# Optimization experiments

Measured on AMD Instinct MI355X. Metric: run time of the kernel, lower is better.

The kernel has to match this reference:

```python
import jax, jax.numpy as jnp
import numpy as np

N, X_DIM, Z_DIM, H = 4096, 256, 128, 512
NUM_ACTIONS = 4
TEMPERATURE = 0.1


def _init_linear(key, fan_in, fan_out):
    kw, kb = jax.random.split(key)
    bound = 1.0 / np.sqrt(fan_in)
    W = jax.random.uniform(kw, (fan_in, fan_out), minval=-bound, maxval=bound, dtype=jnp.float32)
    b = jax.random.uniform(kb, (fan_out,), minval=-bound, maxval=bound, dtype=jnp.float32)
    return W, b


def setup_inputs() -> dict:
    key = jax.random.key(0)
    ks = jax.random.split(key, 9)
    s = jax.random.normal(ks[0], (N, X_DIM), dtype=jnp.float32)
    sp = jax.random.normal(ks[1], (N, X_DIM), dtype=jnp.float32)
    a = jax.random.randint(ks[2], (N,), 0, NUM_ACTIONS)
    a1h = jax.nn.one_hot(a, NUM_ACTIONS, dtype=jnp.float32)
    # phi: x_dim -> 512 -> 512 -> z_dim
    pW0, pb0 = _init_linear(ks[3], X_DIM, H)
    pW1, pb1 = _init_linear(ks[4], H, H)
    pW2, pb2 = _init_linear(ks[5], H, Z_DIM)
    # g: x_dim + 4 -> 512 -> 512 -> z_dim
    gW0, gb0 = _init_linear(ks[6], X_DIM + NUM_ACTIONS, H)
    gW1, gb1 = _init_linear(ks[7], H, H)
    gW2, gb2 = _init_linear(ks[8], H, Z_DIM)
    return {"s": s, "sp": sp, "a1h": a1h,
            "pW0": pW0, "pb0": pb0, "pW1": pW1, "pb1": pb1, "pW2": pW2, "pb2": pb2,
            "gW0": gW0, "gb0": gb0, "gW1": gW1, "gb1": gb1, "gW2": gW2, "gb2": gb2}


def _mlp(x, W0, b0, W1, b1, W2, b2):
    h = jax.nn.relu(x @ W0 + b0)
    h = jax.nn.relu(h @ W1 + b1)
    return h @ W2 + b2


def reference(s, sp, a1h, pW0, pb0, pW1, pb1, pW2, pb2, gW0, gb0, gW1, gb1, gW2, gb2):
    z = _mlp(s, pW0, pb0, pW1, pb1, pW2, pb2)                      # [N, D]
    zpos = _mlp(jnp.concatenate([sp, a1h], axis=-1), gW0, gb0, gW1, gb1, gW2, gb2)  # [N, D]
    # -||z_i - zpos_j||^2 / T via the GEMM trick (avoids the [N,N,D] diff tensor)
    sq_z = jnp.sum(z * z, axis=-1, keepdims=True)                  # [N, 1]
    sq_p = jnp.sum(zpos * zpos, axis=-1)                            # [N]
    logits = -(sq_z + sq_p[None, :] - 2.0 * z @ zpos.T) / TEMPERATURE  # [N, N]
    # cross-entropy with targets = arange(N): diagonal is the positive
    log_probs = jax.nn.log_softmax(logits, axis=-1)
    loss = -jnp.mean(jnp.diagonal(log_probs))
    return loss
```

## Files before the change

### kernel.cpp

```cpp
#include <hip/hip_runtime.h>
#include <math.h>

#define NR 4096
#define ZD 128
#define HD 512
#define NJR 32
#define INV_T 10.0f

typedef __attribute__((ext_vector_type(8))) short bf16x8;
typedef __attribute__((ext_vector_type(4))) short short4v;
typedef __attribute__((ext_vector_type(4))) float f32x4;

typedef const unsigned int __attribute__((address_space(1)))* gas_t;
typedef unsigned int __attribute__((address_space(3)))* las_t;

__device__ __forceinline__ unsigned short f2bf(float f) {
  union { float f; unsigned u; } v; v.f = f;
  unsigned r = v.u + 0x7fff + ((v.u >> 16) & 1);
  return (unsigned short)(r >> 16);
}
__device__ __forceinline__ float bf2f(unsigned short b) {
  union { unsigned u; float f; } v; v.u = ((unsigned)b) << 16;
  return v.f;
}


__global__ __launch_bounds__(256) void prep(
    const float* __restrict__ s, const float* __restrict__ sp,
    const float* __restrict__ a1h,
    unsigned short* __restrict__ Sb, unsigned short* __restrict__ SPb,
    int* __restrict__ aidx,
    const float* __restrict__ pW0, unsigned short* __restrict__ pW0t,
    const float* __restrict__ pW1, unsigned short* __restrict__ pW1t,
    const float* __restrict__ pW2, unsigned short* __restrict__ pW2t,
    const float* __restrict__ gW0, unsigned short* __restrict__ gW0t,
    const float* __restrict__ gW1, unsigned short* __restrict__ gW1t,
    const float* __restrict__ gW2, unsigned short* __restrict__ gW2t,
    float* __restrict__ out) {
  int b = blockIdx.x, tid = threadIdx.x;
  if (b < 16) {
    int r = b * 256 + tid;
    int a = 0;
#pragma unroll
    for (int j = 0; j < 4; ++j) if (a1h[(size_t)r * 4 + j] > 0.5f) a = j;
    aidx[r] = a;
    if (b == 0 && tid == 0) out[0] = 0.f;
    return;
  }
  const int idx8 = tid & 127;
  const int h = idx8 & 1, p = idx8 >> 1, hi = p >> 4, l15 = p & 15;
  if (b < 2064) {
    const float* src = (b < 1040) ? s : sp;
    unsigned short* dst = (b < 1040) ? Sb : SPb;
    int lb = (b < 1040) ? b - 16 : b - 1040;
    int s0 = lb * 2 + (tid >> 7);
    int rf = s0 >> 3, ks = s0 & 7;
    int row = rf * 16 + l15, c0 = ks * 32 + hi * 4 + h * 16;
    float4 v = *(const float4*)&src[(size_t)row * 256 + c0];
    short4v o = { (short)f2bf(v.x), (short)f2bf(v.y), (short)f2bf(v.z), (short)f2bf(v.w) };
    *(short4v*)((char*)dst + (size_t)s0 * 1024 + idx8 * 8) = o;
    return;
  }
  int local = b - 2064;
  const float* W; unsigned short* Wt; int N, ksh;
  if (local < 128)      { W = pW0; Wt = pW0t; N = 512; ksh = 3; }
  else if (local < 384) { W = pW1; Wt = pW1t; N = 512; ksh = 4; local -= 128; }
  else if (local < 448) { W = pW2; Wt = pW2t; N = 128; ksh = 4; local -= 384; }
  else if (local < 576) { W = gW0; Wt = gW0t; N = 512; ksh = 3; local -= 448; }
  else if (local < 832) { W = gW1; Wt = gW1t; N = 512; ksh = 4; local -= 576; }
  else                  { W = gW2; Wt = gW2t; N = 128; ksh = 4; local -= 832; }
  int s0 = local * 2 + (tid >> 7);
  int rf = s0 >> ksh, ks = s0 & ((1 << ksh) - 1);
  int n = rf * 16 + l15, k0 = ks * 32 + hi * 4 + h * 16;
  short4v o = { (short)f2bf(W[(size_t)(k0 + 0) * N + n]),
                (short)f2bf(W[(size_t)(k0 + 1) * N + n]),
                (short)f2bf(W[(size_t)(k0 + 2) * N + n]),
                (short)f2bf(W[(size_t)(k0 + 3) * N + n]) };
  *(short4v*)((char*)Wt + (size_t)s0 * 1024 + idx8 * 8) = o;
}

template <int BM, int K, bool RELU, bool GB, bool SQ>
__global__ __launch_bounds__(256) void gemm_p3(
    const unsigned short* __restrict__ A0, const unsigned short* __restrict__ A1,
    const unsigned short* __restrict__ W0, const unsigned short* __restrict__ W1,
    const float* __restrict__ b0, const float* __restrict__ b1,
    unsigned short* __restrict__ C0, unsigned short* __restrict__ C1,
    float* __restrict__ sqp2, int N,
    const int* __restrict__ aidx, const float* __restrict__ gW0f) {
  constexpr int KS = K >> 5;
  constexpr int NSTEP = K >> 6;
  constexpr int ABYTES = BM * 128;
  constexpr int BBYTES = 8192;
  constexpr int NA = BM >> 5;
  constexpr int WM_FR = BM >> 5;
  constexpr int V = NA + 2;
  __shared__ char lds[3 * (ABYTES + BBYTES)];
  char* AsB = lds;
  char* BsB = lds + 3 * ABYTES;

  const int tid = threadIdx.x, lane = tid & 63, w = tid >> 6;
  const int wm = w >> 1, wn = w & 1;
  const int z = blockIdx.z;
  const char* Ab = (const char*)(z ? A1 : A0);
  const char* Wb = (const char*)(z ? W1 : W0);
  const float* bias = z ? b1 : b0;
  char* Cb = (char*)(z ? C1 : C0);
  const int bm = blockIdx.x * BM, bn = blockIdx.y * 64;
  const int lane16 = lane * 16;

  auto stage = [&](int buf, int st) {
#pragma unroll
    for (int u = 0; u < NA; ++u) {
      const int sl = w * NA + u;
      const char* src = Ab + ((size_t)((bm >> 4) + (sl >> 1)) * KS + st * 2 + (sl & 1)) * 1024 + lane16;
      __builtin_amdgcn_global_load_lds((gas_t)src, (las_t)(AsB + buf * ABYTES + sl * 1024), 16, 0, 0);
    }
#pragma unroll
    for (int u = 0; u < 2; ++u) {
      const int sl = w * 2 + u;
      const char* src = Wb + ((size_t)((bn >> 4) + (sl >> 1)) * KS + st * 2 + (sl & 1)) * 1024 + lane16;
      __builtin_amdgcn_global_load_lds((gas_t)src, (las_t)(BsB + buf * BBYTES + sl * 1024), 16, 0, 0);
    }
  };

  f32x4 acc[WM_FR][2] = {};
  stage(0, 0);
  stage(1, 1);
#pragma unroll
  for (int st = 0; st < NSTEP; ++st) {
    const int buf = st % 3;
    if (st + 2 < NSTEP) {
      stage((st + 2) % 3, st + 2);
      if constexpr (V == 6) asm volatile("s_waitcnt vmcnt(12)" ::: "memory");
      else                  asm volatile("s_waitcnt vmcnt(8)" ::: "memory");
    } else if (st + 1 < NSTEP) {
      if constexpr (V == 6) asm volatile("s_waitcnt vmcnt(6)" ::: "memory");
      else                  asm volatile("s_waitcnt vmcnt(4)" ::: "memory");
    } else {
      asm volatile("s_waitcnt vmcnt(0)" ::: "memory");
    }
    __builtin_amdgcn_s_barrier();
#pragma unroll
    for (int kss = 0; kss < 2; ++kss) {
      bf16x8 af[WM_FR], bfv[2];
#pragma unroll
      for (int i = 0; i < WM_FR; ++i)
        af[i] = *(const bf16x8*)(AsB + buf * ABYTES + ((wm * WM_FR + i) * 2 + kss) * 1024 + lane16);
#pragma unroll
      for (int j = 0; j < 2; ++j)
        bfv[j] = *(const bf16x8*)(BsB + buf * BBYTES + ((wn * 2 + j) * 2 + kss) * 1024 + lane16);
#pragma unroll
      for (int i = 0; i < WM_FR; ++i)
#pragma unroll
        for (int j = 0; j < 2; ++j)
          acc[i][j] = __builtin_amdgcn_mfma_f32_16x16x32_bf16(bfv[j], af[i], acc[i][j], 0, 0, 0);
    }
    __builtin_amdgcn_s_barrier();
  }

  const int l15 = lane & 15, hi = lane >> 4;
  const int NS = N >> 5;
  const int row0 = bm + wm * (BM / 2);
  const int col0 = bn + wn * 32;
  float sq[WM_FR];
  int ar[WM_FR];
#pragma unroll
  for (int i = 0; i < WM_FR; ++i) { sq[i] = 0.f; ar[i] = 0; }
  if (GB && z == 1) {
#pragma unroll
    for (int i = 0; i < WM_FR; ++i) ar[i] = aidx[row0 + i * 16 + l15];
  }
  float4 bi0 = *(const float4*)&bias[col0 + hi * 4];
  float4 bi1 = *(const float4*)&bias[col0 + 16 + hi * 4];
#pragma unroll
  for (int i = 0; i < WM_FR; ++i) {
    const int rfC = (row0 >> 4) + i;
    float v[8] = { acc[i][0][0] + bi0.x, acc[i][0][1] + bi0.y,
                   acc[i][0][2] + bi0.z, acc[i][0][3] + bi0.w,
                   acc[i][1][0] + bi1.x, acc[i][1][1] + bi1.y,
                   acc[i][1][2] + bi1.z, acc[i][1][3] + bi1.w };
    if (GB && z == 1) {
      float4 g0 = *(const float4*)&gW0f[(size_t)(256 + ar[i]) * N + col0 + hi * 4];
      float4 g1 = *(const float4*)&gW0f[(size_t)(256 + ar[i]) * N + col0 + 16 + hi * 4];
      v[0] += g0.x; v[1] += g0.y; v[2] += g0.z; v[3] += g0.w;
      v[4] += g1.x; v[5] += g1.y; v[6] += g1.z; v[7] += g1.w;
    }
    bf16x8 r;
#pragma unroll
    for (int t = 0; t < 8; ++t) {
      float vv = RELU ? fmaxf(v[t], 0.f) : v[t];
      unsigned short cv = f2bf(vv);
      r[t] = (short)cv;
      if (SQ) { float vb = bf2f(cv); sq[i] += vb * vb; }
    }
    *(bf16x8*)(Cb + (size_t)(rfC * NS + (col0 >> 5)) * 1024 + lane16) = r;
  }
  if (SQ && z == 1) {
#pragma unroll
    for (int i = 0; i < WM_FR; ++i) {
      float t = sq[i];
      t += __shfl_xor(t, 16, 64);
      t += __shfl_xor(t, 32, 64);
      if (lane < 16) sqp2[(size_t)(col0 >> 5) * NR + row0 + i * 16 + lane] = t;
    }
  }
}

__global__ __launch_bounds__(256) void logits_fm(
    const unsigned short* __restrict__ Zb, const unsigned short* __restrict__ Zpb,
    const float* __restrict__ sqp2, float* __restrict__ wm_,
    float* __restrict__ wsum, float* __restrict__ wdiag) {
  const int tid = threadIdx.x, lane = tid & 63, w = tid >> 6;
  const int l15 = lane & 15, hi = lane >> 4;
  const int i0 = blockIdx.x * 128, jr = blockIdx.y;
  const int row32 = i0 + w * 32;
  const int jbase = jr * 128;
  const int lane16 = lane * 16;
  const char* Zc = (const char*)Zb;
  const char* Pc = (const char*)Zpb;

  bf16x8 afr[2][4];
#pragma unroll
  for (int rf = 0; rf < 2; ++rf)
#pragma unroll
    for (int ks = 0; ks < 4; ++ks)
      afr[rf][ks] = *(const bf16x8*)(Zc + (size_t)(((row32 >> 4) + rf) * 4 + ks) * 1024 + lane16);

  f32x4 acc[2][8] = {};
#pragma unroll
  for (int jf = 0; jf < 8; ++jf) {
    const size_t js = (size_t)((jbase >> 4) + jf) * 4;
#pragma unroll
    for (int ks = 0; ks < 4; ++ks) {
      bf16x8 bfv = *(const bf16x8*)(Pc + (js + ks) * 1024 + lane16);
      acc[0][jf] = __builtin_amdgcn_mfma_f32_16x16x32_bf16(bfv, afr[0][ks], acc[0][jf], 0, 0, 0);
      acc[1][jf] = __builtin_amdgcn_mfma_f32_16x16x32_bf16(bfv, afr[1][ks], acc[1][jf], 0, 0, 0);
    }
  }

#pragma unroll
  for (int rf = 0; rf < 2; ++rf) {
    const int grow = row32 + rf * 16 + l15;
    float mx = -INFINITY, dd = 0.f;
    bool hasd = false;
#pragma unroll
    for (int jf = 0; jf < 8; ++jf) {
      const int cb = jbase + jf * 16 + hi * 4;
      float4 q0 = *(const float4*)&sqp2[cb];
      float4 q1 = *(const float4*)&sqp2[NR + cb];
      float4 q2 = *(const float4*)&sqp2[2 * NR + cb];
      float4 q3 = *(const float4*)&sqp2[3 * NR + cb];
      float sp[4] = { q0.x + q1.x + q2.x + q3.x, q0.y + q1.y + q2.y + q3.y,
                      q0.z + q1.z + q2.z + q3.z, q0.w + q1.w + q2.w + q3.w };
#pragma unroll
      for (int e = 0; e < 4; ++e) {
        float lv = (2.f * acc[rf][jf][e] - sp[e]) * INV_T;
        acc[rf][jf][e] = lv;
        mx = fmaxf(mx, lv);
        if (cb + e == grow) { dd = lv; hasd = true; }
      }
    }
    mx = fmaxf(mx, __shfl_xor(mx, 16, 64));
    mx = fmaxf(mx, __shfl_xor(mx, 32, 64));
    float sum = 0.f;
#pragma unroll
    for (int jf = 0; jf < 8; ++jf)
#pragma unroll
      for (int e = 0; e < 4; ++e) sum += __expf(acc[rf][jf][e] - mx);
    sum += __shfl_xor(sum, 16, 64);
    sum += __shfl_xor(sum, 32, 64);
    if (hi == 0) {
      wm_[(size_t)jr * NR + grow] = mx;
      wsum[(size_t)jr * NR + grow] = sum;
    }
    if (hasd) wdiag[grow] = dd;
  }
}

__global__ __launch_bounds__(256) void finalize(const float* __restrict__ wm,
    const float* __restrict__ wsum, const float* __restrict__ wdiag,
    float* __restrict__ out) {
  int r = blockIdx.x * 256 + threadIdx.x;
  float mm = wm[r];
  float ss = wsum[r];
#pragma unroll
  for (int p = 1; p < NJR; ++p) {
    float mo = wm[(size_t)p * NR + r];
    float so = wsum[(size_t)p * NR + r];
    float mn = fmaxf(mm, mo);
    ss = ss * __expf(mm - mn) + so * __expf(mo - mn);
    mm = mn;
  }
  float loss_r = mm + logf(ss) - wdiag[r];
  float v = loss_r;
#pragma unroll
  for (int off = 32; off; off >>= 1) v += __shfl_xor(v, off, 64);
  __shared__ float partial[4];
  if ((threadIdx.x & 63) == 0) partial[threadIdx.x >> 6] = v;
  __syncthreads();
  if (threadIdx.x == 0)
    atomicAdd(out, (partial[0] + partial[1] + partial[2] + partial[3]) * (1.0f / (float)NR));
}

extern "C" void kernel_launch(void* const* d_in, const int* in_sizes, int n_in,
                              void* d_out, int out_size, void* d_ws, size_t ws_size,
                              hipStream_t stream) {
  const float* s   = (const float*)d_in[0];
  const float* sp  = (const float*)d_in[1];
  const float* a1h = (const float*)d_in[2];
  const float* pW0 = (const float*)d_in[3];
  const float* pb0 = (const float*)d_in[4];
  const float* pW1 = (const float*)d_in[5];
  const float* pb1 = (const float*)d_in[6];
  const float* pW2 = (const float*)d_in[7];
  const float* pb2 = (const float*)d_in[8];
  const float* gW0 = (const float*)d_in[9];
  const float* gb0 = (const float*)d_in[10];
  const float* gW1 = (const float*)d_in[11];
  const float* gb1 = (const float*)d_in[12];
  const float* gW2 = (const float*)d_in[13];
  const float* gb2 = (const float*)d_in[14];

  char* p = (char*)d_ws;
  unsigned short* Sb   = (unsigned short*)p; p += (size_t)NR * 256 * 2;
  unsigned short* SPb  = (unsigned short*)p; p += (size_t)NR * 256 * 2;
  unsigned short* H1   = (unsigned short*)p; p += (size_t)2 * NR * HD * 2;
  unsigned short* H2   = (unsigned short*)p; p += (size_t)2 * NR * HD * 2;
  unsigned short* Zall = (unsigned short*)p; p += (size_t)2 * NR * ZD * 2;
  unsigned short* pW0t = (unsigned short*)p; p += (size_t)256 * 512 * 2;
  unsigned short* pW1t = (unsigned short*)p; p += (size_t)512 * 512 * 2;
  unsigned short* pW2t = (unsigned short*)p; p += (size_t)512 * 128 * 2;
  unsigned short* gW0t = (unsigned short*)p; p += (size_t)256 * 512 * 2;
  unsigned short* gW1t = (unsigned short*)p; p += (size_t)512 * 512 * 2;
  unsigned short* gW2t = (unsigned short*)p; p += (size_t)512 * 128 * 2;
  float* sqp2 = (float*)p; p += (size_t)4 * NR * 4;
  float* wm   = (float*)p; p += (size_t)NJR * NR * 4;
  float* wsm  = (float*)p; p += (size_t)NJR * NR * 4;
  float* wdg  = (float*)p; p += (size_t)NR * 4;
  int*   aidx = (int*)p;  p += (size_t)NR * 4;

  unsigned short* H1g = H1 + (size_t)NR * HD;
  unsigned short* H2g = H2 + (size_t)NR * HD;
  unsigned short* Zb  = Zall;
  unsigned short* Zpb = Zall + (size_t)NR * ZD;

  dim3 blk(256);
  prep<<<2960, blk, 0, stream>>>(s, sp, a1h, Sb, SPb, aidx,
                                 pW0, pW0t, pW1, pW1t, pW2, pW2t,
                                 gW0, gW0t, gW1, gW1t, gW2, gW2t,
                                 (float*)d_out);

  gemm_p3<128, 256, true, true, false><<<dim3(32, 8, 2), blk, 0, stream>>>(
      Sb, SPb, pW0t, gW0t, pb0, gb0, H1, H1g, nullptr, 512, aidx, gW0);
  gemm_p3<128, 512, true, false, false><<<dim3(32, 8, 2), blk, 0, stream>>>(
      H1, H1g, pW1t, gW1t, pb1, gb1, H2, H2g, nullptr, 512, nullptr, nullptr);
  gemm_p3<64, 512, false, false, true><<<dim3(64, 2, 2), blk, 0, stream>>>(
      H2, H2g, pW2t, gW2t, pb2, gb2, Zb, Zpb, sqp2, 128, nullptr, nullptr);

  logits_fm<<<dim3(NR / 128, NJR), blk, 0, stream>>>(Zb, Zpb, sqp2, wm, wsm, wdg);
  finalize<<<NR / 256, blk, 0, stream>>>(wm, wsm, wdg, (float*)d_out);
}
```

Before: 54.47 us.

## Fuse finalize into logits kernel via atomic last-block reduction and stage Zp in LDS

```diff
diff --git a/kernel.cpp b/kernel.cpp
--- a/kernel.cpp
+++ b/kernel.cpp
@@ -2,10 +2,10 @@
 #include <math.h>
 
 #define NR 4096
-#define ZD 128
 #define HD 512
 #define NJR 32
 #define INV_T 10.0f
+#define DONE_FINAL 1024
 
 typedef __attribute__((ext_vector_type(8))) short bf16x8;
 typedef __attribute__((ext_vector_type(4))) short short4v;
@@ -36,7 +36,7 @@
     const float* __restrict__ gW0, unsigned short* __restrict__ gW0t,
     const float* __restrict__ gW1, unsigned short* __restrict__ gW1t,
     const float* __restrict__ gW2, unsigned short* __restrict__ gW2t,
-    float* __restrict__ out) {
+    unsigned* __restrict__ done, float* __restrict__ out) {
   int b = blockIdx.x, tid = threadIdx.x;
   if (b < 16) {
     int r = b * 256 + tid;
@@ -45,6 +45,7 @@
     for (int j = 0; j < 4; ++j) if (a1h[(size_t)r * 4 + j] > 0.5f) a = j;
     aidx[r] = a;
     if (b == 0 && tid == 0) out[0] = 0.f;
+    if (b == 1) { for (int i = tid; i < 1025; i += 256) done[i] = 0; }
     return;
   }
   const int idx8 = tid & 127;
@@ -206,37 +207,62 @@
   }
 }
 
-__global__ __launch_bounds__(256) void logits_fm(
+__global__ __launch_bounds__(256) void logits_fin(
     const unsigned short* __restrict__ Zb, const unsigned short* __restrict__ Zpb,
-    const float* __restrict__ sqp2, float* __restrict__ wm_,
-    float* __restrict__ wsum, float* __restrict__ wdiag) {
+    const float* __restrict__ sqp4, float* __restrict__ wm_,
+    float* __restrict__ wsum, float* __restrict__ wdiag,
+    unsigned* __restrict__ done, float* __restrict__ out) {
+  __shared__ __align__(1024) char Ps[32768];
+  __shared__ int hid;
+  __shared__ float fpart[4];
   const int tid = threadIdx.x, lane = tid & 63, w = tid >> 6;
   const int l15 = lane & 15, hi = lane >> 4;
-  const int i0 = blockIdx.x * 128, jr = blockIdx.y;
+  const int bx = blockIdx.x, jr = blockIdx.y;
+  const int i0 = bx * 128;
   const int row32 = i0 + w * 32;
   const int jbase = jr * 128;
   const int lane16 = lane * 16;
   const char* Zc = (const char*)Zb;
   const char* Pc = (const char*)Zpb;
 
+#pragma unroll
+  for (int u = 0; u < 8; ++u) {
+    const int sl = w * 8 + u;
+    __builtin_amdgcn_global_load_lds(
+        (gas_t)(Pc + ((size_t)(jbase >> 4) * 4 + sl) * 1024 + lane16),
+        (las_t)(Ps + sl * 1024), 16, 0, 0);
+  }
   bf16x8 afr[2][4];
 #pragma unroll
   for (int rf = 0; rf < 2; ++rf)
 #pragma unroll
     for (int ks = 0; ks < 4; ++ks)
       afr[rf][ks] = *(const bf16x8*)(Zc + (size_t)(((row32 >> 4) + rf) * 4 + ks) * 1024 + lane16);
+  f32x4 spq[8];
+#pragma unroll
+  for (int jf = 0; jf < 8; ++jf) {
+    const int cb = jbase + jf * 16 + hi * 4;
+    float4 q0 = *(const float4*)&sqp4[cb];
+    float4 q1 = *(const float4*)&sqp4[NR + cb];
+    float4 q2 = *(const float4*)&sqp4[2 * NR + cb];
+    float4 q3 = *(const float4*)&sqp4[3 * NR + cb];
+    spq[jf][0] = q0.x + q1.x + q2.x + q3.x;
+    spq[jf][1] = q0.y + q1.y + q2.y + q3.y;
+    spq[jf][2] = q0.z + q1.z + q2.z + q3.z;
+    spq[jf][3] = q0.w + q1.w + q2.w + q3.w;
+  }
+  asm volatile("s_waitcnt vmcnt(0)" ::: "memory");
+  __syncthreads();
 
   f32x4 acc[2][8] = {};
 #pragma unroll
-  for (int jf = 0; jf < 8; ++jf) {
-    const size_t js = (size_t)((jbase >> 4) + jf) * 4;
-#pragma unroll
-    for (int ks = 0; ks < 4; ++ks) {
-      bf16x8 bfv = *(const bf16x8*)(Pc + (js + ks) * 1024 + lane16);
+  for (int ks = 0; ks < 4; ++ks)
+#pragma unroll
+    for (int jf = 0; jf < 8; ++jf) {
+      bf16x8 bfv = *(const bf16x8*)(Ps + (jf * 4 + ks) * 1024 + lane16);
       acc[0][jf] = __builtin_amdgcn_mfma_f32_16x16x32_bf16(bfv, afr[0][ks], acc[0][jf], 0, 0, 0);
       acc[1][jf] = __builtin_amdgcn_mfma_f32_16x16x32_bf16(bfv, afr[1][ks], acc[1][jf], 0, 0, 0);
     }
-  }
 
 #pragma unroll
   for (int rf = 0; rf < 2; ++rf) {
@@ -246,15 +272,9 @@
 #pragma unroll
     for (int jf = 0; jf < 8; ++jf) {
       const int cb = jbase + jf * 16 + hi * 4;
-      float4 q0 = *(const float4*)&sqp2[cb];
-      float4 q1 = *(const float4*)&sqp2[NR + cb];
-      float4 q2 = *(const float4*)&sqp2[2 * NR + cb];
-      float4 q3 = *(const float4*)&sqp2[3 * NR + cb];
-      float sp[4] = { q0.x + q1.x + q2.x + q3.x, q0.y + q1.y + q2.y + q3.y,
-                      q0.z + q1.z + q2.z + q3.z, q0.w + q1.w + q2.w + q3.w };
 #pragma unroll
       for (int e = 0; e < 4; ++e) {
-        float lv = (2.f * acc[rf][jf][e] - sp[e]) * INV_T;
+        float lv = (2.f * acc[rf][jf][e] - spq[jf][e]) * INV_T;
         acc[rf][jf][e] = lv;
         mx = fmaxf(mx, lv);
         if (cb + e == grow) { dd = lv; hasd = true; }
@@ -275,31 +295,47 @@
     }
     if (hasd) wdiag[grow] = dd;
   }
-}
-
-__global__ __launch_bounds__(256) void finalize(const float* __restrict__ wm,
-    const float* __restrict__ wsum, const float* __restrict__ wdiag,
-    float* __restrict__ out) {
-  int r = blockIdx.x * 256 + threadIdx.x;
-  float mm = wm[r];
-  float ss = wsum[r];
-#pragma unroll
-  for (int p = 1; p < NJR; ++p) {
-    float mo = wm[(size_t)p * NR + r];
-    float so = wsum[(size_t)p * NR + r];
-    float mn = fmaxf(mm, mo);
-    ss = ss * __expf(mm - mn) + so * __expf(mo - mn);
-    mm = mn;
-  }
-  float loss_r = mm + logf(ss) - wdiag[r];
-  float v = loss_r;
-#pragma unroll
-  for (int off = 32; off; off >>= 1) v += __shfl_xor(v, off, 64);
-  __shared__ float partial[4];
-  if ((threadIdx.x & 63) == 0) partial[threadIdx.x >> 6] = v;
+
   __syncthreads();
-  if (threadIdx.x == 0)
-    atomicAdd(out, (partial[0] + partial[1] + partial[2] + partial[3]) * (1.0f / (float)NR));
+  if (tid == 0) {
+    hid = -1;
+    const int bid = jr * 32 + bx;
+    unsigned old = __hip_atomic_fetch_add(&done[(bid & 63) * 16], 1u,
+                                          __ATOMIC_ACQ_REL, __HIP_MEMORY_SCOPE_AGENT);
+    if (old == 15u) {
+      unsigned f = __hip_atomic_fetch_add(&done[DONE_FINAL], 1u,
+                                          __ATOMIC_ACQ_REL, __HIP_MEMORY_SCOPE_AGENT);
+      if (f >= 48u) {
+        while (__hip_atomic_load(&done[DONE_FINAL], __ATOMIC_ACQUIRE,
+                                 __HIP_MEMORY_SCOPE_AGENT) < 64u)
+          __builtin_amdgcn_s_sleep(16);
+        hid = (int)(f - 48u);
+      }
+    }
+  }
+  __syncthreads();
+  if (hid < 0) return;
+
+  {
+    const int r = hid * 256 + tid;
+    float mm = wm_[r];
+    float ss = wsum[r];
+#pragma unroll
+    for (int p = 1; p < NJR; ++p) {
+      float mo = wm_[(size_t)p * NR + r];
+      float so = wsum[(size_t)p * NR + r];
+      float mn = fmaxf(mm, mo);
+      ss = ss * __expf(mm - mn) + so * __expf(mo - mn);
+      mm = mn;
+    }
+    float v = mm + logf(ss) - wdiag[r];
+#pragma unroll
+    for (int off = 32; off; off >>= 1) v += __shfl_xor(v, off, 64);
+    if (lane == 0) fpart[w] = v;
+    __syncthreads();
+    if (tid == 0)
+      atomicAdd(out, (fpart[0] + fpart[1] + fpart[2] + fpart[3]) * (1.0f / (float)NR));
+  }
 }
 
 extern "C" void kernel_launch(void* const* d_in, const int* in_sizes, int n_in,
@@ -326,37 +362,38 @@
   unsigned short* SPb  = (unsigned short*)p; p += (size_t)NR * 256 * 2;
   unsigned short* H1   = (unsigned short*)p; p += (size_t)2 * NR * HD * 2;
   unsigned short* H2   = (unsigned short*)p; p += (size_t)2 * NR * HD * 2;
-  unsigned short* Zall = (unsigned short*)p; p += (size_t)2 * NR * ZD * 2;
+  unsigned short* Zall = (unsigned short*)p; p += (size_t)2 * NR * 128 * 2;
   unsigned short* pW0t = (unsigned short*)p; p += (size_t)256 * 512 * 2;
   unsigned short* pW1t = (unsigned short*)p; p += (size_t)512 * 512 * 2;
   unsigned short* pW2t = (unsigned short*)p; p += (size_t)512 * 128 * 2;
   unsigned short* gW0t = (unsigned short*)p; p += (size_t)256 * 512 * 2;
   unsigned short* gW1t = (unsigned short*)p; p += (size_t)512 * 512 * 2;
   unsigned short* gW2t = (unsigned short*)p; p += (size_t)512 * 128 * 2;
-  float* sqp2 = (float*)p; p += (size_t)4 * NR * 4;
+  float* sqp4 = (float*)p; p += (size_t)4 * NR * 4;
   float* wm   = (float*)p; p += (size_t)NJR * NR * 4;
   float* wsm  = (float*)p; p += (size_t)NJR * NR * 4;
   float* wdg  = (float*)p; p += (size_t)NR * 4;
   int*   aidx = (int*)p;  p += (size_t)NR * 4;
+  unsigned* done = (unsigned*)p; p += 8192;
 
   unsigned short* H1g = H1 + (size_t)NR * HD;
   unsigned short* H2g = H2 + (size_t)NR * HD;
   unsigned short* Zb  = Zall;
-  unsigned short* Zpb = Zall + (size_t)NR * ZD;
+  unsigned short* Zpb = Zall + (size_t)NR * 128;
 
   dim3 blk(256);
   prep<<<2960, blk, 0, stream>>>(s, sp, a1h, Sb, SPb, aidx,
                                  pW0, pW0t, pW1, pW1t, pW2, pW2t,
                                  gW0, gW0t, gW1, gW1t, gW2, gW2t,
-                                 (float*)d_out);
+                                 done, (float*)d_out);
 
   gemm_p3<128, 256, true, true, false><<<dim3(32, 8, 2), blk, 0, stream>>>(
       Sb, SPb, pW0t, gW0t, pb0, gb0, H1, H1g, nullptr, 512, aidx, gW0);
   gemm_p3<128, 512, true, false, false><<<dim3(32, 8, 2), blk, 0, stream>>>(
       H1, H1g, pW1t, gW1t, pb1, gb1, H2, H2g, nullptr, 512, nullptr, nullptr);
   gemm_p3<64, 512, false, false, true><<<dim3(64, 2, 2), blk, 0, stream>>>(
-      H2, H2g, pW2t, gW2t, pb2, gb2, Zb, Zpb, sqp2, 128, nullptr, nullptr);
-
-  logits_fm<<<dim3(NR / 128, NJR), blk, 0, stream>>>(Zb, Zpb, sqp2, wm, wsm, wdg);
-  finalize<<<NR / 256, blk, 0, stream>>>(wm, wsm, wdg, (float*)d_out);
-}
+      H2, H2g, pW2t, gW2t, pb2, gb2, Zb, Zpb, sqp4, 128, nullptr, nullptr);
+
+  logits_fin<<<dim3(32, 32), blk, 0, stream>>>(Zb, Zpb, sqp4, wm, wsm, wdg,
+                                               done, (float*)d_out);
+}
```

Result: slower. 69.80 us (+28.1%).

## Overlap weight conversion with first GEMM and stream logits with online softmax

Applied to the files above, without the earlier changes.

```diff
diff --git a/kernel.cpp b/kernel.cpp
--- a/kernel.cpp
+++ b/kernel.cpp
@@ -2,9 +2,8 @@
 #include <math.h>
 
 #define NR 4096
-#define ZD 128
 #define HD 512
-#define NJR 32
+#define NJR 16
 #define INV_T 10.0f
 
 typedef __attribute__((ext_vector_type(8))) short bf16x8;
@@ -25,50 +24,10 @@
 }
 
 
-__global__ __launch_bounds__(256) void prep(
-    const float* __restrict__ s, const float* __restrict__ sp,
-    const float* __restrict__ a1h,
-    unsigned short* __restrict__ Sb, unsigned short* __restrict__ SPb,
-    int* __restrict__ aidx,
-    const float* __restrict__ pW0, unsigned short* __restrict__ pW0t,
-    const float* __restrict__ pW1, unsigned short* __restrict__ pW1t,
-    const float* __restrict__ pW2, unsigned short* __restrict__ pW2t,
-    const float* __restrict__ gW0, unsigned short* __restrict__ gW0t,
-    const float* __restrict__ gW1, unsigned short* __restrict__ gW1t,
-    const float* __restrict__ gW2, unsigned short* __restrict__ gW2t,
-    float* __restrict__ out) {
-  int b = blockIdx.x, tid = threadIdx.x;
-  if (b < 16) {
-    int r = b * 256 + tid;
-    int a = 0;
-#pragma unroll
-    for (int j = 0; j < 4; ++j) if (a1h[(size_t)r * 4 + j] > 0.5f) a = j;
-    aidx[r] = a;
-    if (b == 0 && tid == 0) out[0] = 0.f;
-    return;
-  }
+__device__ __forceinline__ void wt_unit(int local, int tid, const float* W,
+                                        unsigned short* Wt, int N, int ksh) {
   const int idx8 = tid & 127;
   const int h = idx8 & 1, p = idx8 >> 1, hi = p >> 4, l15 = p & 15;
-  if (b < 2064) {
-    const float* src = (b < 1040) ? s : sp;
-    unsigned short* dst = (b < 1040) ? Sb : SPb;
-    int lb = (b < 1040) ? b - 16 : b - 1040;
-    int s0 = lb * 2 + (tid >> 7);
-    int rf = s0 >> 3, ks = s0 & 7;
-    int row = rf * 16 + l15, c0 = ks * 32 + hi * 4 + h * 16;
-    float4 v = *(const float4*)&src[(size_t)row * 256 + c0];
-    short4v o = { (short)f2bf(v.x), (short)f2bf(v.y), (short)f2bf(v.z), (short)f2bf(v.w) };
-    *(short4v*)((char*)dst + (size_t)s0 * 1024 + idx8 * 8) = o;
-    return;
-  }
-  int local = b - 2064;
-  const float* W; unsigned short* Wt; int N, ksh;
-  if (local < 128)      { W = pW0; Wt = pW0t; N = 512; ksh = 3; }
-  else if (local < 384) { W = pW1; Wt = pW1t; N = 512; ksh = 4; local -= 128; }
-  else if (local < 448) { W = pW2; Wt = pW2t; N = 128; ksh = 4; local -= 384; }
-  else if (local < 576) { W = gW0; Wt = gW0t; N = 512; ksh = 3; local -= 448; }
-  else if (local < 832) { W = gW1; Wt = gW1t; N = 512; ksh = 4; local -= 576; }
-  else                  { W = gW2; Wt = gW2t; N = 128; ksh = 4; local -= 832; }
   int s0 = local * 2 + (tid >> 7);
   int rf = s0 >> ksh, ks = s0 & ((1 << ksh) - 1);
   int n = rf * 16 + l15, k0 = ks * 32 + hi * 4 + h * 16;
@@ -79,14 +38,69 @@
   *(short4v*)((char*)Wt + (size_t)s0 * 1024 + idx8 * 8) = o;
 }
 
-template <int BM, int K, bool RELU, bool GB, bool SQ>
+__global__ __launch_bounds__(256) void prep(
+    const float* __restrict__ s, const float* __restrict__ sp,
+    const float* __restrict__ a1h,
+    unsigned short* __restrict__ Sb, unsigned short* __restrict__ SPb,
+    int* __restrict__ aidx, float* __restrict__ sqp,
+    const float* __restrict__ pW0, unsigned short* __restrict__ pW0t,
+    const float* __restrict__ gW0, unsigned short* __restrict__ gW0t,
+    float* __restrict__ out) {
+  const int tid = threadIdx.x;
+  for (int u = blockIdx.x; u < 2320; u += 580) {
+    if (u < 16) {
+      int r = u * 256 + tid;
+      int a = 0;
+#pragma unroll
+      for (int j = 0; j < 4; ++j) if (a1h[(size_t)r * 4 + j] > 0.5f) a = j;
+      aidx[r] = a;
+      sqp[r] = 0.f;
+      if (u == 0 && tid == 0) out[0] = 0.f;
+      continue;
+    }
+    if (u < 2064) {
+      const int b = u;
+      const float* src = (b < 1040) ? s : sp;
+      unsigned short* dst = (b < 1040) ? Sb : SPb;
+      int lb = (b < 1040) ? b - 16 : b - 1040;
+      const int idx8 = tid & 127;
+      const int h = idx8 & 1, p = idx8 >> 1, hi = p >> 4, l15 = p & 15;
+      int s0 = lb * 2 + (tid >> 7);
+      int rf = s0 >> 3, ks = s0 & 7;
+      int row = rf * 16 + l15, c0 = ks * 32 + hi * 4 + h * 16;
+      float4 v = *(const float4*)&src[(size_t)row * 256 + c0];
+      short4v o = { (short)f2bf(v.x), (short)f2bf(v.y), (short)f2bf(v.z), (short)f2bf(v.w) };
+      *(short4v*)((char*)dst + (size_t)s0 * 1024 + idx8 * 8) = o;
+      continue;
+    }
+    int local = u - 2064;
+    if (local < 128) wt_unit(local, tid, pW0, pW0t, 512, 3);
+    else             wt_unit(local - 128, tid, gW0, gW0t, 512, 3);
+  }
+}
+
+template <int BM, int K, bool RELU, bool GB, bool SQ, bool RIDERS>
 __global__ __launch_bounds__(256) void gemm_p3(
     const unsigned short* __restrict__ A0, const unsigned short* __restrict__ A1,
     const unsigned short* __restrict__ W0, const unsigned short* __restrict__ W1,
     const float* __restrict__ b0, const float* __restrict__ b1,
     unsigned short* __restrict__ C0, unsigned short* __restrict__ C1,
-    float* __restrict__ sqp2, int N,
-    const int* __restrict__ aidx, const float* __restrict__ gW0f) {
+    float* __restrict__ sqp, int N, int gx, int gy,
+    const int* __restrict__ aidx, const float* __restrict__ gW0f,
+    const float* __restrict__ rpW1, unsigned short* __restrict__ rpW1t,
+    const float* __restrict__ rpW2, unsigned short* __restrict__ rpW2t,
+    const float* __restrict__ rgW1, unsigned short* __restrict__ rgW1t,
+    const float* __restrict__ rgW2, unsigned short* __restrict__ rgW2t) {
+  const int tid = threadIdx.x;
+  const int ngemm = gx * gy * 2;
+  if (RIDERS && (int)blockIdx.x >= ngemm) {
+    int local = blockIdx.x - ngemm;
+    if (local < 256)      wt_unit(local, tid, rpW1, rpW1t, 512, 4);
+    else if (local < 320) wt_unit(local - 256, tid, rpW2, rpW2t, 128, 4);
+    else if (local < 576) wt_unit(local - 320, tid, rgW1, rgW1t, 512, 4);
+    else                  wt_unit(local - 576, tid, rgW2, rgW2t, 128, 4);
+    return;
+  }
   constexpr int KS = K >> 5;
   constexpr int NSTEP = K >> 6;
   constexpr int ABYTES = BM * 128;
@@ -98,14 +112,15 @@
   char* AsB = lds;
   char* BsB = lds + 3 * ABYTES;
 
-  const int tid = threadIdx.x, lane = tid & 63, w = tid >> 6;
+  const int bid = blockIdx.x;
+  const int bx = bid % gx, by = (bid / gx) % gy, z = bid / (gx * gy);
+  const int lane = tid & 63, w = tid >> 6;
   const int wm = w >> 1, wn = w & 1;
-  const int z = blockIdx.z;
   const char* Ab = (const char*)(z ? A1 : A0);
   const char* Wb = (const char*)(z ? W1 : W0);
   const float* bias = z ? b1 : b0;
   char* Cb = (char*)(z ? C1 : C0);
-  const int bm = blockIdx.x * BM, bn = blockIdx.y * 64;
+  const int bm = bx * BM, bn = by * 64;
   const int lane16 = lane * 16;
 
   auto stage = [&](int buf, int st) {
@@ -201,20 +216,20 @@
       float t = sq[i];
       t += __shfl_xor(t, 16, 64);
       t += __shfl_xor(t, 32, 64);
-      if (lane < 16) sqp2[(size_t)(col0 >> 5) * NR + row0 + i * 16 + lane] = t;
+      if (lane < 16) atomicAdd(&sqp[row0 + i * 16 + lane], t);
     }
   }
 }
 
 __global__ __launch_bounds__(256) void logits_fm(
     const unsigned short* __restrict__ Zb, const unsigned short* __restrict__ Zpb,
-    const float* __restrict__ sqp2, float* __restrict__ wm_,
+    const float* __restrict__ sqp, float* __restrict__ wm_,
     float* __restrict__ wsum, float* __restrict__ wdiag) {
   const int tid = threadIdx.x, lane = tid & 63, w = tid >> 6;
   const int l15 = lane & 15, hi = lane >> 4;
   const int i0 = blockIdx.x * 128, jr = blockIdx.y;
   const int row32 = i0 + w * 32;
-  const int jbase = jr * 128;
+  const int jbase = jr * 256;
   const int lane16 = lane * 16;
   const char* Zc = (const char*)Zb;
   const char* Pc = (const char*)Zpb;
@@ -226,54 +241,67 @@
     for (int ks = 0; ks < 4; ++ks)
       afr[rf][ks] = *(const bf16x8*)(Zc + (size_t)(((row32 >> 4) + rf) * 4 + ks) * 1024 + lane16);
 
-  f32x4 acc[2][8] = {};
-#pragma unroll
-  for (int jf = 0; jf < 8; ++jf) {
-    const size_t js = (size_t)((jbase >> 4) + jf) * 4;
-#pragma unroll
-    for (int ks = 0; ks < 4; ++ks) {
-      bf16x8 bfv = *(const bf16x8*)(Pc + (js + ks) * 1024 + lane16);
-      acc[0][jf] = __builtin_amdgcn_mfma_f32_16x16x32_bf16(bfv, afr[0][ks], acc[0][jf], 0, 0, 0);
-      acc[1][jf] = __builtin_amdgcn_mfma_f32_16x16x32_bf16(bfv, afr[1][ks], acc[1][jf], 0, 0, 0);
+  float m[2] = {-INFINITY, -INFINITY}, sv[2] = {0.f, 0.f}, dd[2] = {0.f, 0.f};
+  bool hasd[2] = {false, false};
+  const int grow0 = row32 + l15, grow1 = row32 + 16 + l15;
+
+#pragma unroll
+  for (int g = 0; g < 4; ++g) {
+    f32x4 acc[2][4] = {};
+#pragma unroll
+    for (int ks = 0; ks < 4; ++ks)
+#pragma unroll
+      for (int q = 0; q < 4; ++q) {
+        bf16x8 bfv = *(const bf16x8*)(Pc + (size_t)(((jbase >> 4) + g * 4 + q) * 4 + ks) * 1024 + lane16);
+        acc[0][q] = __builtin_amdgcn_mfma_f32_16x16x32_bf16(bfv, afr[0][ks], acc[0][q], 0, 0, 0);
+        acc[1][q] = __builtin_amdgcn_mfma_f32_16x16x32_bf16(bfv, afr[1][ks], acc[1][q], 0, 0, 0);
+      }
+    f32x4 spq[4];
+#pragma unroll
+    for (int q = 0; q < 4; ++q)
+      spq[q] = *(const f32x4*)&sqp[jbase + (g * 4 + q) * 16 + hi * 4];
+#pragma unroll
+    for (int rf = 0; rf < 2; ++rf) {
+      const int grow = rf ? grow1 : grow0;
+      float lv[16];
+      float lmax = -INFINITY;
+#pragma unroll
+      for (int q = 0; q < 4; ++q)
+#pragma unroll
+        for (int e = 0; e < 4; ++e) {
+          const int j = jbase + (g * 4 + q) * 16 + hi * 4 + e;
+          float x = (2.f * acc[rf][q][e] - spq[q][e]) * INV_T;
+          lv[q * 4 + e] = x;
+          lmax = fmaxf(lmax, x);
+          if (j == grow) { dd[rf] = x; hasd[rf] = true; }
+        }
+      float mn = fmaxf(m[rf], lmax);
+      float sc = __expf(m[rf] - mn);
+      float ls = 0.f;
+#pragma unroll
+      for (int t = 0; t < 16; ++t) ls += __expf(lv[t] - mn);
+      sv[rf] = sv[rf] * sc + ls;
+      m[rf] = mn;
     }
   }
 
 #pragma unroll
   for (int rf = 0; rf < 2; ++rf) {
-    const int grow = row32 + rf * 16 + l15;
-    float mx = -INFINITY, dd = 0.f;
-    bool hasd = false;
-#pragma unroll
-    for (int jf = 0; jf < 8; ++jf) {
-      const int cb = jbase + jf * 16 + hi * 4;
-      float4 q0 = *(const float4*)&sqp2[cb];
-      float4 q1 = *(const float4*)&sqp2[NR + cb];
-      float4 q2 = *(const float4*)&sqp2[2 * NR + cb];
-      float4 q3 = *(const float4*)&sqp2[3 * NR + cb];
-      float sp[4] = { q0.x + q1.x + q2.x + q3.x, q0.y + q1.y + q2.y + q3.y,
-                      q0.z + q1.z + q2.z + q3.z, q0.w + q1.w + q2.w + q3.w };
-#pragma unroll
-      for (int e = 0; e < 4; ++e) {
-        float lv = (2.f * acc[rf][jf][e] - sp[e]) * INV_T;
-        acc[rf][jf][e] = lv;
-        mx = fmaxf(mx, lv);
-        if (cb + e == grow) { dd = lv; hasd = true; }
-      }
-    }
-    mx = fmaxf(mx, __shfl_xor(mx, 16, 64));
-    mx = fmaxf(mx, __shfl_xor(mx, 32, 64));
-    float sum = 0.f;
-#pragma unroll
-    for (int jf = 0; jf < 8; ++jf)
-#pragma unroll
-      for (int e = 0; e < 4; ++e) sum += __expf(acc[rf][jf][e] - mx);
-    sum += __shfl_xor(sum, 16, 64);
-    sum += __shfl_xor(sum, 32, 64);
+    const int grow = rf ? grow1 : grow0;
+    float mm = m[rf], ss = sv[rf];
+#pragma unroll
+    for (int off = 16; off <= 32; off <<= 1) {
+      float mo = __shfl_xor(mm, off, 64);
+      float so = __shfl_xor(ss, off, 64);
+      float mn = fmaxf(mm, mo);
+      ss = ss * __expf(mm - mn) + so * __expf(mo - mn);
+      mm = mn;
+    }
     if (hi == 0) {
-      wm_[(size_t)jr * NR + grow] = mx;
-      wsum[(size_t)jr * NR + grow] = sum;
-    }
-    if (hasd) wdiag[grow] = dd;
+      wm_[(size_t)jr * NR + grow] = mm;
+      wsum[(size_t)jr * NR + grow] = ss;
+    }
+    if (hasd[rf]) wdiag[grow] = dd[rf];
   }
 }
 
@@ -326,14 +354,14 @@
   unsigned short* SPb  = (unsigned short*)p; p += (size_t)NR * 256 * 2;
   unsigned short* H1   = (unsigned short*)p; p += (size_t)2 * NR * HD * 2;
   unsigned short* H2   = (unsigned short*)p; p += (size_t)2 * NR * HD * 2;
-  unsigned short* Zall = (unsigned short*)p; p += (size_t)2 * NR * ZD * 2;
+  unsigned short* Zall = (unsigned short*)p; p += (size_t)2 * NR * 128 * 2;
   unsigned short* pW0t = (unsigned short*)p; p += (size_t)256 * 512 * 2;
   unsigned short* pW1t = (unsigned short*)p; p += (size_t)512 * 512 * 2;
   unsigned short* pW2t = (unsigned short*)p; p += (size_t)512 * 128 * 2;
   unsigned short* gW0t = (unsigned short*)p; p += (size_t)256 * 512 * 2;
   unsigned short* gW1t = (unsigned short*)p; p += (size_t)512 * 512 * 2;
   unsigned short* gW2t = (unsigned short*)p; p += (size_t)512 * 128 * 2;
-  float* sqp2 = (float*)p; p += (size_t)4 * NR * 4;
+  float* sqp  = (float*)p; p += (size_t)NR * 4;
   float* wm   = (float*)p; p += (size_t)NJR * NR * 4;
   float* wsm  = (float*)p; p += (size_t)NJR * NR * 4;
   float* wdg  = (float*)p; p += (size_t)NR * 4;
@@ -342,21 +370,24 @@
   unsigned short* H1g = H1 + (size_t)NR * HD;
   unsigned short* H2g = H2 + (size_t)NR * HD;
   unsigned short* Zb  = Zall;
-  unsigned short* Zpb = Zall + (size_t)NR * ZD;
+  unsigned short* Zpb = Zall + (size_t)NR * 128;
 
   dim3 blk(256);
-  prep<<<2960, blk, 0, stream>>>(s, sp, a1h, Sb, SPb, aidx,
-                                 pW0, pW0t, pW1, pW1t, pW2, pW2t,
-                                 gW0, gW0t, gW1, gW1t, gW2, gW2t,
-                                 (float*)d_out);
-
-  gemm_p3<128, 256, true, true, false><<<dim3(32, 8, 2), blk, 0, stream>>>(
-      Sb, SPb, pW0t, gW0t, pb0, gb0, H1, H1g, nullptr, 512, aidx, gW0);
-  gemm_p3<128, 512, true, false, false><<<dim3(32, 8, 2), blk, 0, stream>>>(
-      H1, H1g, pW1t, gW1t, pb1, gb1, H2, H2g, nullptr, 512, nullptr, nullptr);
-  gemm_p3<64, 512, false, false, true><<<dim3(64, 2, 2), blk, 0, stream>>>(
-      H2, H2g, pW2t, gW2t, pb2, gb2, Zb, Zpb, sqp2, 128, nullptr, nullptr);
-
-  logits_fm<<<dim3(NR / 128, NJR), blk, 0, stream>>>(Zb, Zpb, sqp2, wm, wsm, wdg);
+  prep<<<580, blk, 0, stream>>>(s, sp, a1h, Sb, SPb, aidx, sqp,
+                                pW0, pW0t, gW0, gW0t, (float*)d_out);
+
+  gemm_p3<128, 256, true, true, false, true><<<1152, blk, 0, stream>>>(
+      Sb, SPb, pW0t, gW0t, pb0, gb0, H1, H1g, nullptr, 512, 32, 8, aidx, gW0,
+      pW1, pW1t, pW2, pW2t, gW1, gW1t, gW2, gW2t);
+
+  gemm_p3<128, 512, true, false, false, false><<<512, blk, 0, stream>>>(
+      H1, H1g, pW1t, gW1t, pb1, gb1, H2, H2g, nullptr, 512, 32, 8, nullptr, nullptr,
+      nullptr, nullptr, nullptr, nullptr, nullptr, nullptr, nullptr, nullptr);
+
+  gemm_p3<64, 512, false, false, true, false><<<256, blk, 0, stream>>>(
+      H2, H2g, pW2t, gW2t, pb2, gb2, Zb, Zpb, sqp, 128, 64, 2, nullptr, nullptr,
+      nullptr, nullptr, nullptr, nullptr, nullptr, nullptr, nullptr, nullptr);
+
+  logits_fm<<<dim3(32, NJR), blk, 0, stream>>>(Zb, Zpb, sqp, wm, wsm, wdg);
   finalize<<<NR / 256, blk, 0, stream>>>(wm, wsm, wdg, (float*)d_out);
 }
```

After: 46.18 us (median of 2 runs). -15.2%, faster.
